# Kernel tuning notes

Measured on AMD Instinct MI355X. Metric: run time of the kernel, lower is better.

Reference implementation:

```python
import jax, jax.numpy as jnp
import numpy as np

D = 200          # in_feat == out_feat
N = 20000        # num nodes
E = 320000       # num edges
R = 512          # num relation types


def setup_inputs() -> dict:
    key = jax.random.key(0)
    ks = jax.random.split(key, 12)
    # glorot-ish init scale for params
    def glorot(k, shape):
        fan = shape[0] + shape[1]
        return jax.random.normal(k, shape, dtype=jnp.float32) * jnp.sqrt(2.0 / fan)
    return {
        "node": jax.random.normal(ks[0], (N, D), dtype=jnp.float32),
        "rel": jax.random.normal(ks[1], (R, D), dtype=jnp.float32),
        "norm": jax.random.uniform(ks[2], (N, 1), dtype=jnp.float32),
        "fre": jax.random.uniform(ks[3], (E,), dtype=jnp.float32),
        "w_triplet": glorot(ks[4], (3 * D, D)),
        "w_quad": glorot(ks[5], (D, D)),
        "loop_weight": glorot(ks[6], (D, D)),
        "evolve_loop_weight": glorot(ks[7], (D, D)),
        "edge_src": jax.random.randint(ks[8], (E,), 0, N, dtype=jnp.int64).astype(jnp.int32),
        "edge_dst": jax.random.randint(ks[9], (E,), 0, N, dtype=jnp.int64).astype(jnp.int32),
        "edge_type": jax.random.randint(ks[10], (E,), 0, R, dtype=jnp.int64).astype(jnp.int32),
    }


def reference(node, rel, norm, fre, w_triplet, w_quad, loop_weight,
              evolve_loop_weight, edge_src, edge_dst, edge_type):
    n = node.shape[0]
    d = node.shape[1]
    # gather per-edge features
    src_h = node[edge_src]            # [E, D]
    dst_h = node[edge_dst]            # [E, D]
    rel_emb = rel[edge_type]          # [E, D]
    # quads_msg_func: concat([src,rel,dst]) @ w_triplet, split to avoid [E,3D] concat
    W_s, W_r, W_d = w_triplet[:d], w_triplet[d:2 * d], w_triplet[2 * d:]
    triplet = src_h @ W_s + rel_emb @ W_r + dst_h @ W_d   # [E, D]
    a = (triplet + fre[:, None]) @ w_quad                 # [E, D]
    a = jax.nn.leaky_relu(a, negative_slope=0.01)
    # edge softmax over incoming edges per destination node (per channel)
    seg_max = jax.ops.segment_max(a, edge_dst, num_segments=n)   # [N, D]
    ex = jnp.exp(a - seg_max[edge_dst])
    seg_sum = jax.ops.segment_sum(ex, edge_dst, num_segments=n)  # [N, D]
    att = ex / seg_sum[edge_dst]
    # weighted message aggregation + per-node norm
    h = jax.ops.segment_sum(att * triplet, edge_dst, num_segments=n)
    h = h * norm
    # self-loop: loop_weight where in_degree > 0, else evolve_loop_weight
    deg = jax.ops.segment_sum(jnp.ones((edge_dst.shape[0],), dtype=jnp.float32),
                              edge_dst, num_segments=n)
    loop_msg = jnp.where((deg > 0)[:, None],
                         node @ loop_weight,
                         node @ evolve_loop_weight)
    return jax.nn.relu(h + loop_msg)
```

## Files before the change

### kernel.cpp

```cpp
#include <hip/hip_runtime.h>
#include <hip/hip_bf16.h>
#include <cstdint>
#include <cstddef>

#define DD 200
#define NN 20000
#define EE 320000
#define RRR 512
#define KP 256
#define KREAL 224
#define MT 157
#define NT 10
#define RMT 4
#define RNT 4
#define NBLK_NODE (MT * NT)

typedef __attribute__((ext_vector_type(8))) short bf16x8;
typedef __attribute__((ext_vector_type(4))) float f32x4;

__device__ __forceinline__ float bf2f_lo(unsigned int u) { return __uint_as_float(u << 16); }
__device__ __forceinline__ float bf2f_hi(unsigned int u) { return __uint_as_float(u & 0xffff0000u); }
__device__ __forceinline__ unsigned short f2bf(float f) {
  unsigned int x = __float_as_uint(f);
  return (unsigned short)((x + 0x7fffu + ((x >> 16) & 1u)) >> 16);
}
__device__ __forceinline__ unsigned int f2bf2(float a, float b) {
  return (unsigned int)f2bf(a) | ((unsigned int)f2bf(b) << 16);
}
__device__ __forceinline__ void gl_lds16(const unsigned short* g, unsigned short* l) {
  __builtin_amdgcn_global_load_lds(
      (const __attribute__((address_space(1))) void*)g,
      (__attribute__((address_space(3))) void*)l, 16, 0, 0);
}

__global__ __launch_bounds__(256) void kA(const float* __restrict__ wt, const float* __restrict__ wq,
                                          const float* __restrict__ lw, const float* __restrict__ elw,
                                          unsigned short* __restrict__ Bt,
                                          unsigned short* __restrict__ BtRel,
                                          float* __restrict__ cq, int* __restrict__ degcur) {
  int b = blockIdx.x, t = threadIdx.x;
  if (b < 200) {
    int k = b, j = t;
    if (j >= DD) return;
    const float* w0 = wt + (size_t)k * DD;
    const float* w1 = wt + (size_t)(2 * DD + k) * DD;
    const float* w2 = wt + (size_t)(DD + k) * DD;
    float s0 = 0.f, s1 = 0.f, s2 = 0.f;
    for (int i = 0; i < DD; ++i) {
      float q = wq[i * DD + j];
      s0 = fmaf(w0[i], q, s0);
      s1 = fmaf(w1[i], q, s1);
      s2 = fmaf(w2[i], q, s2);
    }
    Bt[(2 * j) * KP + k]       = f2bf(w0[j]);
    Bt[(2 * j + 1) * KP + k]   = f2bf(s0);
    Bt[(400 + 2 * j) * KP + k] = f2bf(w1[j]);
    Bt[(401 + 2 * j) * KP + k] = f2bf(s1);
    Bt[(800 + 2 * j) * KP + k] = f2bf(lw[k * DD + j]);
    Bt[(801 + 2 * j) * KP + k] = f2bf(elw[k * DD + j]);
    BtRel[(2 * j) * KP + k]     = f2bf(w2[j]);
    BtRel[(2 * j + 1) * KP + k] = f2bf(s2);
  } else if (b == 200) {
    int j = t; if (j >= DD) return;
    float s = 0.f;
    for (int i = 0; i < DD; ++i) s += wq[i * DD + j];
    cq[j] = s;
  } else if (b < 397) {
    int idx = (b - 201) * 256 + t;
    if (idx < 1792 * 28) {
      int col = idx / 28, kk = idx % 28;
      ((unsigned int*)Bt)[col * 128 + 100 + kk] = 0;
    }
  } else {
    int idx = (b - 397) * 256 + t;
    if (idx < 2 * NN) degcur[idx] = 0;
  }
}

__global__ __launch_bounds__(128) void k_prep(const float* __restrict__ node, const float* __restrict__ rel,
                                              const int* __restrict__ dst,
                                              unsigned int* __restrict__ Au, unsigned int* __restrict__ Arelu,
                                              int* __restrict__ deg) {
  int b = blockIdx.x, t = threadIdx.x;
  if (b < NN) {
    unsigned v = 0;
    if (t < 100) { float2 f = ((const float2*)(node + (size_t)b * DD))[t]; v = f2bf2(f.x, f.y); }
    Au[(size_t)b * 128 + t] = v;
  } else if (b < NN + RRR) {
    int r = b - NN; unsigned v = 0;
    if (t < 100) { float2 f = ((const float2*)(rel + (size_t)r * DD))[t]; v = f2bf2(f.x, f.y); }
    Arelu[(size_t)r * 128 + t] = v;
  } else {
    int e = (b - NN - RRR) * 128 + t;
    if (e < EE) atomicAdd(&deg[dst[e]], 1);
  }
}

__global__ __launch_bounds__(1024) void k_scan(const int* __restrict__ deg, int* __restrict__ offs) {
  __shared__ int wsum[16];
  __shared__ int carry_s;
  int tid = threadIdx.x, lane = tid & 63, wv = tid >> 6;
  if (tid == 0) carry_s = 0;
  __syncthreads();
  const int4* deg4 = (const int4*)deg;
  int4* offs4 = (int4*)offs;
  for (int base = 0; base < 5000; base += 1024) {
    int idx = base + tid;
    int4 v = make_int4(0, 0, 0, 0);
    if (idx < 5000) v = deg4[idx];
    int tsum = v.x + v.y + v.z + v.w;
    int x = tsum;
#pragma unroll
    for (int off = 1; off < 64; off <<= 1) {
      int y = __shfl_up(x, off, 64);
      if (lane >= off) x += y;
    }
    if (lane == 63) wsum[wv] = x;
    __syncthreads();
    if (wv == 0) {
      int w = (lane < 16) ? wsum[lane] : 0;
#pragma unroll
      for (int off = 1; off < 16; off <<= 1) {
        int y = __shfl_up(w, off, 64);
        if (lane >= off) w += y;
      }
      if (lane < 16) wsum[lane] = w;
    }
    __syncthreads();
    int pre = carry_s + ((wv > 0) ? wsum[wv - 1] : 0) + x - tsum;
    if (idx < 5000) {
      int a = pre, b = pre + v.x, c = b + v.y, d = c + v.z;
      offs4[idx] = make_int4(a, b, c, d);
    }
    __syncthreads();
    if (tid == 1023) carry_s += wsum[15];
    __syncthreads();
  }
  if (tid == 0) offs[NN] = carry_s;
}

__global__ __launch_bounds__(256) void k_gemm(const unsigned short* __restrict__ A,
                                              const unsigned short* __restrict__ Bt,
                                              unsigned short* __restrict__ NT2u,
                                              const unsigned short* __restrict__ Arel,
                                              const unsigned short* __restrict__ BtRel,
                                              unsigned short* __restrict__ RelPu) {
  __shared__ unsigned short As[128 * 32];
  __shared__ unsigned short Bs[128 * 32];
  bool isrel = blockIdx.x >= NBLK_NODE;
  int bid, ntn;
  const unsigned short *Ag, *Bg;
  if (!isrel) { bid = blockIdx.x; ntn = NT; Ag = A; Bg = Bt; }
  else        { bid = blockIdx.x - NBLK_NODE; ntn = RNT; Ag = Arel; Bg = BtRel; }
  int mt = bid / ntn, nt = bid % ntn;
  int t = threadIdx.x, lane = t & 63, wv = t >> 6;
  int lr = lane & 15, k8 = lane >> 4;
  int wm = (wv >> 1) * 64, wn = (wv & 1) * 64;
  int sr = wv * 16 + (lane >> 2);
  int sc = lane & 3;
  f32x4 acc[4][4] = {};
  Ag += (size_t)(mt * 128) * KP;
  Bg += (size_t)(nt * 128) * KP;
  for (int kk = 0; kk < KREAL; kk += 32) {
#pragma unroll
    for (int i = 0; i < 2; ++i) {
      int row = i * 64 + sr;
      int gcol = kk + ((sc ^ (row & 3)) << 3);
      gl_lds16(Ag + (size_t)row * KP + gcol, As + i * 2048 + wv * 512);
      gl_lds16(Bg + (size_t)row * KP + gcol, Bs + i * 2048 + wv * 512);
    }
    __syncthreads();
    bf16x8 af[4], bfr[4];
#pragma unroll
    for (int mi = 0; mi < 4; ++mi) {
      int row = wm + mi * 16 + lr;
      af[mi] = *(const bf16x8*)(As + row * 32 + ((k8 ^ (row & 3)) << 3));
      int col = wn + mi * 16 + lr;
      bfr[mi] = *(const bf16x8*)(Bs + col * 32 + ((k8 ^ (col & 3)) << 3));
    }
#pragma unroll
    for (int mi = 0; mi < 4; ++mi)
#pragma unroll
      for (int ni = 0; ni < 4; ++ni)
        acc[mi][ni] = __builtin_amdgcn_mfma_f32_16x16x32_bf16(af[mi], bfr[ni], acc[mi][ni], 0, 0, 0);
    __syncthreads();
  }
  int rb = k8 * 4;
#pragma unroll
  for (int mi = 0; mi < 4; ++mi)
#pragma unroll
    for (int ni = 0; ni < 4; ++ni) {
      int col = nt * 128 + wn + ni * 16 + lr;
      if (!isrel) {
        if (col < 1200) {
          int g = col / 400, w = col - g * 400;
          unsigned short* dst = NT2u + (size_t)g * NN * 400 + w;
#pragma unroll
          for (int r = 0; r < 4; ++r) {
            int row = mt * 128 + wm + mi * 16 + rb + r;
            if (row < NN) dst[(size_t)row * 400] = f2bf(acc[mi][ni][r]);
          }
        }
      } else {
        if (col < 400) {
#pragma unroll
          for (int r = 0; r < 4; ++r) {
            int row = mt * 128 + wm + mi * 16 + rb + r;
            RelPu[(size_t)row * 400 + col] = f2bf(acc[mi][ni][r]);
          }
        }
      }
    }
}

__global__ __launch_bounds__(256) void k_scatter(const int* __restrict__ src, const int* __restrict__ dst,
                                                 const int* __restrict__ typ, const float* __restrict__ fre,
                                                 const int* __restrict__ offs, int* __restrict__ cursor,
                                                 int* __restrict__ spk, float* __restrict__ sfre) {
  int e = blockIdx.x * 256 + threadIdx.x;
  if (e >= EE) return;
  int d = dst[e];
  int p = offs[d] + atomicAdd(&cursor[d], 1);
  spk[p] = src[e] | (typ[e] << 15);
  sfre[p] = fre[e];
}

__global__ __launch_bounds__(128) void k_agg(const uint2* __restrict__ GS2,
                                             const uint2* __restrict__ GD2,
                                             const uint2* __restrict__ GL2,
                                             const uint2* __restrict__ Rel2,
                                             const float2* __restrict__ cq2,
                                             const float* __restrict__ norm,
                                             const int* __restrict__ offs,
                                             const int* __restrict__ spk, const float* __restrict__ sfre,
                                             float* __restrict__ out) {
  int n = blockIdx.x;
  int j2 = threadIdx.x;
  if (j2 >= 100) return;
  int e0 = offs[n], e1 = offs[n + 1];
  uint2 dp = GD2[(size_t)n * 100 + j2];
  float xd0 = bf2f_lo(dp.x), xq0 = bf2f_hi(dp.x);
  float xd1 = bf2f_lo(dp.y), xq1 = bf2f_hi(dp.y);
  float2 cqv = cq2[j2];
  float s0 = 0.f, s1 = 0.f, num0 = 0.f, num1 = 0.f;
  int i = e0;
  for (; i + 4 <= e1; i += 4) {
    int p0 = spk[i], p1 = spk[i + 1], p2 = spk[i + 2], p3 = spk[i + 3];
    float f0 = sfre[i], f1 = sfre[i + 1], f2 = sfre[i + 2], f3 = sfre[i + 3];
    uint2 sA = GS2[((unsigned)p0 & 0x7fffu) * 100u + j2];
    uint2 sB = GS2[((unsigned)p1 & 0x7fffu) * 100u + j2];
    uint2 sC = GS2[((unsigned)p2 & 0x7fffu) * 100u + j2];
    uint2 sD = GS2[((unsigned)p3 & 0x7fffu) * 100u + j2];
    uint2 rA = Rel2[((unsigned)p0 >> 15) * 100u + j2];
    uint2 rB = Rel2[((unsigned)p1 >> 15) * 100u + j2];
    uint2 rC = Rel2[((unsigned)p2 >> 15) * 100u + j2];
    uint2 rD = Rel2[((unsigned)p3 >> 15) * 100u + j2];
#define DO_EDGE(SP, RP, F)                                                    \
    {                                                                         \
      float t0 = bf2f_lo(SP.x) + bf2f_lo(RP.x) + xd0;                         \
      float a0 = bf2f_hi(SP.x) + bf2f_hi(RP.x) + fmaf(F, cqv.x, xq0);         \
      float t1 = bf2f_lo(SP.y) + bf2f_lo(RP.y) + xd1;                         \
      float a1 = bf2f_hi(SP.y) + bf2f_hi(RP.y) + fmaf(F, cqv.y, xq1);         \
      a0 = fmaxf(a0, 0.01f * a0); a1 = fmaxf(a1, 0.01f * a1);                 \
      float ev0 = __expf(a0), ev1 = __expf(a1);                               \
      s0 += ev0; num0 = fmaf(ev0, t0, num0);                                  \
      s1 += ev1; num1 = fmaf(ev1, t1, num1);                                  \
    }
    DO_EDGE(sA, rA, f0)
    DO_EDGE(sB, rB, f1)
    DO_EDGE(sC, rC, f2)
    DO_EDGE(sD, rD, f3)
  }
  for (; i < e1; ++i) {
    int p = spk[i]; float f = sfre[i];
    uint2 sp = GS2[((unsigned)p & 0x7fffu) * 100u + j2];
    uint2 rp = Rel2[((unsigned)p >> 15) * 100u + j2];
    DO_EDGE(sp, rp, f)
  }
#undef DO_EDGE
  uint2 lp = GL2[(size_t)n * 100 + j2];
  float o0, o1;
  if (e1 > e0) {
    float nm = norm[n];
    o0 = (num0 / s0) * nm + bf2f_lo(lp.x);
    o1 = (num1 / s1) * nm + bf2f_lo(lp.y);
  } else {
    o0 = bf2f_hi(lp.x);
    o1 = bf2f_hi(lp.y);
  }
  ((float2*)(out + (size_t)n * DD))[j2] = make_float2(fmaxf(o0, 0.f), fmaxf(o1, 0.f));
}

extern "C" void kernel_launch(void* const* d_in, const int* in_sizes, int n_in,
                              void* d_out, int out_size, void* d_ws, size_t ws_size,
                              hipStream_t stream) {
  const float* node = (const float*)d_in[0];
  const float* rel  = (const float*)d_in[1];
  const float* norm = (const float*)d_in[2];
  const float* fre  = (const float*)d_in[3];
  const float* wt   = (const float*)d_in[4];
  const float* wq   = (const float*)d_in[5];
  const float* lw   = (const float*)d_in[6];
  const float* elw  = (const float*)d_in[7];
  const int* esrc = (const int*)d_in[8];
  const int* edst = (const int*)d_in[9];
  const int* etyp = (const int*)d_in[10];
  float* out = (float*)d_out;

  char* p = (char*)d_ws;
  auto carve = [&](size_t bytes) -> char* {
    char* r = p; p += (bytes + 255) & ~(size_t)255; return r;
  };
  unsigned short* A     = (unsigned short*)carve((size_t)(MT * 128) * KP * 2);
  unsigned short* Arel  = (unsigned short*)carve((size_t)RRR * KP * 2);
  unsigned short* BtAll = (unsigned short*)carve((size_t)(1280 + 512) * KP * 2);
  unsigned short* NT2   = (unsigned short*)carve((size_t)3 * NN * 400 * 2);
  unsigned short* RelP  = (unsigned short*)carve((size_t)RRR * 400 * 2);
  float* cq   = (float*)carve((size_t)DD * 4);
  int* degcur = (int*)carve((size_t)2 * NN * 4);
  int* offs   = (int*)carve((size_t)(NN + 1) * 4);
  int* spk    = (int*)carve((size_t)EE * 4);
  float* sfre = (float*)carve((size_t)EE * 4);

  unsigned short* Bt    = BtAll;
  unsigned short* BtRel = BtAll + (size_t)1280 * KP;
  int* deg    = degcur;
  int* cursor = degcur + NN;

  const uint2* GS2 = (const uint2*)NT2;
  const uint2* GD2 = GS2 + (size_t)NN * 100;
  const uint2* GL2 = GS2 + (size_t)2 * NN * 100;

  kA<<<554, 256, 0, stream>>>(wt, wq, lw, elw, Bt, BtRel, cq, degcur);
  k_prep<<<NN + RRR + (EE + 127) / 128, 128, 0, stream>>>(node, rel, edst,
                                                          (unsigned int*)A, (unsigned int*)Arel, deg);
  k_scan<<<1, 1024, 0, stream>>>(deg, offs);
  k_gemm<<<NBLK_NODE + RMT * RNT, 256, 0, stream>>>(A, Bt, NT2, Arel, BtRel, RelP);
  k_scatter<<<(EE + 255) / 256, 256, 0, stream>>>(esrc, edst, etyp, fre, offs, cursor,
                                                  spk, sfre);
  k_agg<<<NN, 128, 0, stream>>>(GS2, GD2, GL2, (const uint2*)RelP, (const float2*)cq,
                                norm, offs, spk, sfre, out);
}
```

Baseline: 144.1 us.

## Merge prep kernels, single-pass scan, pack edge records, deepen agg unroll

Merges the weight-prep and node/rel conversion kernels into one launch, with two rows per 256-thread block, and replaces the zeroing of degree counters with a memset. The scan now does a single pass, each thread handling five int4 chunks, instead of looping with a carried sum. Edge source/type and fre are packed into one int2 record. The aggregation loop is unrolled to 8 edges with all loads issued first to raise memory-level parallelism, and the constant dst term is pulled out of the per-edge sum. Scatter is also launched before the GEMM. This reduces launch count and serial scan latency, at the cost of more registers in the aggregation kernel.

```diff
diff --git a/kernel.cpp b/kernel.cpp
--- a/kernel.cpp
+++ b/kernel.cpp
@@ -15,6 +15,13 @@
 #define RNT 4
 #define NBLK_NODE (MT * NT)
 
+#define PB_NODE 10000
+#define PB_REL  (PB_NODE + 256)
+#define PB_HIST (PB_REL + 1250)
+#define PB_W    (PB_HIST + 200)
+#define PB_CQ   (PB_W + 1)
+#define PB_PAD  (PB_CQ + 196)
+
 typedef __attribute__((ext_vector_type(8))) short bf16x8;
 typedef __attribute__((ext_vector_type(4))) float f32x4;
 
@@ -33,14 +40,32 @@
       (__attribute__((address_space(3))) void*)l, 16, 0, 0);
 }
 
-__global__ __launch_bounds__(256) void kA(const float* __restrict__ wt, const float* __restrict__ wq,
-                                          const float* __restrict__ lw, const float* __restrict__ elw,
-                                          unsigned short* __restrict__ Bt,
-                                          unsigned short* __restrict__ BtRel,
-                                          float* __restrict__ cq, int* __restrict__ degcur) {
+__global__ __launch_bounds__(256) void kPrep(const float* __restrict__ node, const float* __restrict__ rel,
+                                             const int* __restrict__ dst,
+                                             const float* __restrict__ wt, const float* __restrict__ wq,
+                                             const float* __restrict__ lw, const float* __restrict__ elw,
+                                             unsigned int* __restrict__ Au, unsigned int* __restrict__ Arelu,
+                                             int* __restrict__ deg,
+                                             unsigned short* __restrict__ Bt, unsigned short* __restrict__ BtRel,
+                                             float* __restrict__ cq) {
   int b = blockIdx.x, t = threadIdx.x;
-  if (b < 200) {
-    int k = b, j = t;
+  if (b < PB_NODE) {
+    int h = t >> 7, tt = t & 127;
+    int n = b * 2 + h;
+    unsigned v = 0;
+    if (tt < 100) { float2 f = ((const float2*)(node + (size_t)n * DD))[tt]; v = f2bf2(f.x, f.y); }
+    Au[(size_t)n * 128 + tt] = v;
+  } else if (b < PB_REL) {
+    int h = t >> 7, tt = t & 127;
+    int r = (b - PB_NODE) * 2 + h;
+    unsigned v = 0;
+    if (tt < 100) { float2 f = ((const float2*)(rel + (size_t)r * DD))[tt]; v = f2bf2(f.x, f.y); }
+    Arelu[(size_t)r * 128 + tt] = v;
+  } else if (b < PB_HIST) {
+    int e = (b - PB_REL) * 256 + t;
+    if (e < EE) atomicAdd(&deg[dst[e]], 1);
+  } else if (b < PB_W) {
+    int k = b - PB_HIST, j = t;
     if (j >= DD) return;
     const float* w0 = wt + (size_t)k * DD;
     const float* w1 = wt + (size_t)(2 * DD + k) * DD;
@@ -60,83 +85,59 @@
     Bt[(801 + 2 * j) * KP + k] = f2bf(elw[k * DD + j]);
     BtRel[(2 * j) * KP + k]     = f2bf(w2[j]);
     BtRel[(2 * j + 1) * KP + k] = f2bf(s2);
-  } else if (b == 200) {
+  } else if (b < PB_CQ) {
     int j = t; if (j >= DD) return;
     float s = 0.f;
     for (int i = 0; i < DD; ++i) s += wq[i * DD + j];
     cq[j] = s;
-  } else if (b < 397) {
-    int idx = (b - 201) * 256 + t;
-    if (idx < 1792 * 28) {
-      int col = idx / 28, kk = idx % 28;
-      ((unsigned int*)Bt)[col * 128 + 100 + kk] = 0;
-    }
   } else {
-    int idx = (b - 397) * 256 + t;
-    if (idx < 2 * NN) degcur[idx] = 0;
-  }
-}
-
-__global__ __launch_bounds__(128) void k_prep(const float* __restrict__ node, const float* __restrict__ rel,
-                                              const int* __restrict__ dst,
-                                              unsigned int* __restrict__ Au, unsigned int* __restrict__ Arelu,
-                                              int* __restrict__ deg) {
-  int b = blockIdx.x, t = threadIdx.x;
-  if (b < NN) {
-    unsigned v = 0;
-    if (t < 100) { float2 f = ((const float2*)(node + (size_t)b * DD))[t]; v = f2bf2(f.x, f.y); }
-    Au[(size_t)b * 128 + t] = v;
-  } else if (b < NN + RRR) {
-    int r = b - NN; unsigned v = 0;
-    if (t < 100) { float2 f = ((const float2*)(rel + (size_t)r * DD))[t]; v = f2bf2(f.x, f.y); }
-    Arelu[(size_t)r * 128 + t] = v;
-  } else {
-    int e = (b - NN - RRR) * 128 + t;
-    if (e < EE) atomicAdd(&deg[dst[e]], 1);
+    int idx = (b - PB_CQ) * 256 + t;
+    ((unsigned int*)Bt)[(idx / 28) * 128 + 100 + idx % 28] = 0;
   }
 }
 
 __global__ __launch_bounds__(1024) void k_scan(const int* __restrict__ deg, int* __restrict__ offs) {
   __shared__ int wsum[16];
-  __shared__ int carry_s;
   int tid = threadIdx.x, lane = tid & 63, wv = tid >> 6;
-  if (tid == 0) carry_s = 0;
-  __syncthreads();
   const int4* deg4 = (const int4*)deg;
   int4* offs4 = (int4*)offs;
-  for (int base = 0; base < 5000; base += 1024) {
-    int idx = base + tid;
-    int4 v = make_int4(0, 0, 0, 0);
-    if (idx < 5000) v = deg4[idx];
-    int tsum = v.x + v.y + v.z + v.w;
-    int x = tsum;
-#pragma unroll
-    for (int off = 1; off < 64; off <<= 1) {
-      int y = __shfl_up(x, off, 64);
-      if (lane >= off) x += y;
-    }
-    if (lane == 63) wsum[wv] = x;
-    __syncthreads();
-    if (wv == 0) {
-      int w = (lane < 16) ? wsum[lane] : 0;
-#pragma unroll
-      for (int off = 1; off < 16; off <<= 1) {
-        int y = __shfl_up(w, off, 64);
-        if (lane >= off) w += y;
-      }
-      if (lane < 16) wsum[lane] = w;
-    }
-    __syncthreads();
-    int pre = carry_s + ((wv > 0) ? wsum[wv - 1] : 0) + x - tsum;
+  int4 v[5]; int ps[5]; int tsum = 0;
+#pragma unroll
+  for (int c = 0; c < 5; ++c) {
+    int idx = tid * 5 + c;
+    v[c] = (idx < 5000) ? deg4[idx] : make_int4(0, 0, 0, 0);
+    ps[c] = tsum;
+    tsum += v[c].x + v[c].y + v[c].z + v[c].w;
+  }
+  int x = tsum;
+#pragma unroll
+  for (int off = 1; off < 64; off <<= 1) {
+    int y = __shfl_up(x, off, 64);
+    if (lane >= off) x += y;
+  }
+  if (lane == 63) wsum[wv] = x;
+  __syncthreads();
+  if (wv == 0) {
+    int w = (lane < 16) ? wsum[lane] : 0;
+#pragma unroll
+    for (int off = 1; off < 16; off <<= 1) {
+      int y = __shfl_up(w, off, 64);
+      if (lane >= off) w += y;
+    }
+    if (lane < 16) wsum[lane] = w;
+  }
+  __syncthreads();
+  int pre = ((wv > 0) ? wsum[wv - 1] : 0) + x - tsum;
+#pragma unroll
+  for (int c = 0; c < 5; ++c) {
+    int idx = tid * 5 + c;
     if (idx < 5000) {
-      int a = pre, b = pre + v.x, c = b + v.y, d = c + v.z;
-      offs4[idx] = make_int4(a, b, c, d);
-    }
-    __syncthreads();
-    if (tid == 1023) carry_s += wsum[15];
-    __syncthreads();
-  }
-  if (tid == 0) offs[NN] = carry_s;
+      int a = pre + ps[c];
+      int bq = a + v[c].x, cc = bq + v[c].y, d = cc + v[c].z;
+      offs4[idx] = make_int4(a, bq, cc, d);
+    }
+  }
+  if (tid == 0) offs[NN] = wsum[15];
 }
 
 __global__ __launch_bounds__(256) void k_gemm(const unsigned short* __restrict__ A,
@@ -216,13 +217,12 @@
 __global__ __launch_bounds__(256) void k_scatter(const int* __restrict__ src, const int* __restrict__ dst,
                                                  const int* __restrict__ typ, const float* __restrict__ fre,
                                                  const int* __restrict__ offs, int* __restrict__ cursor,
-                                                 int* __restrict__ spk, float* __restrict__ sfre) {
+                                                 int2* __restrict__ erec) {
   int e = blockIdx.x * 256 + threadIdx.x;
   if (e >= EE) return;
   int d = dst[e];
   int p = offs[d] + atomicAdd(&cursor[d], 1);
-  spk[p] = src[e] | (typ[e] << 15);
-  sfre[p] = fre[e];
+  erec[p] = make_int2(src[e] | (typ[e] << 15), __float_as_int(fre[e]));
 }
 
 __global__ __launch_bounds__(128) void k_agg(const uint2* __restrict__ GS2,
@@ -232,7 +232,7 @@
                                              const float2* __restrict__ cq2,
                                              const float* __restrict__ norm,
                                              const int* __restrict__ offs,
-                                             const int* __restrict__ spk, const float* __restrict__ sfre,
+                                             const int2* __restrict__ erec,
                                              float* __restrict__ out) {
   int n = blockIdx.x;
   int j2 = threadIdx.x;
@@ -243,47 +243,55 @@
   float xd1 = bf2f_lo(dp.y), xq1 = bf2f_hi(dp.y);
   float2 cqv = cq2[j2];
   float s0 = 0.f, s1 = 0.f, num0 = 0.f, num1 = 0.f;
+#define DO_EDGE(SP, RP, FI)                                                   \
+  {                                                                           \
+    float F = __int_as_float(FI);                                             \
+    float t0 = bf2f_lo(SP.x) + bf2f_lo(RP.x);                                 \
+    float a0 = bf2f_hi(SP.x) + bf2f_hi(RP.x) + fmaf(F, cqv.x, xq0);           \
+    float t1 = bf2f_lo(SP.y) + bf2f_lo(RP.y);                                 \
+    float a1 = bf2f_hi(SP.y) + bf2f_hi(RP.y) + fmaf(F, cqv.y, xq1);           \
+    a0 = fmaxf(a0, 0.01f * a0); a1 = fmaxf(a1, 0.01f * a1);                   \
+    float ev0 = __expf(a0), ev1 = __expf(a1);                                 \
+    s0 += ev0; num0 = fmaf(ev0, t0, num0);                                    \
+    s1 += ev1; num1 = fmaf(ev1, t1, num1);                                    \
+  }
   int i = e0;
-  for (; i + 4 <= e1; i += 4) {
-    int p0 = spk[i], p1 = spk[i + 1], p2 = spk[i + 2], p3 = spk[i + 3];
-    float f0 = sfre[i], f1 = sfre[i + 1], f2 = sfre[i + 2], f3 = sfre[i + 3];
-    uint2 sA = GS2[((unsigned)p0 & 0x7fffu) * 100u + j2];
-    uint2 sB = GS2[((unsigned)p1 & 0x7fffu) * 100u + j2];
-    uint2 sC = GS2[((unsigned)p2 & 0x7fffu) * 100u + j2];
-    uint2 sD = GS2[((unsigned)p3 & 0x7fffu) * 100u + j2];
-    uint2 rA = Rel2[((unsigned)p0 >> 15) * 100u + j2];
-    uint2 rB = Rel2[((unsigned)p1 >> 15) * 100u + j2];
-    uint2 rC = Rel2[((unsigned)p2 >> 15) * 100u + j2];
-    uint2 rD = Rel2[((unsigned)p3 >> 15) * 100u + j2];
-#define DO_EDGE(SP, RP, F)                                                    \
-    {                                                                         \
-      float t0 = bf2f_lo(SP.x) + bf2f_lo(RP.x) + xd0;                         \
-      float a0 = bf2f_hi(SP.x) + bf2f_hi(RP.x) + fmaf(F, cqv.x, xq0);         \
-      float t1 = bf2f_lo(SP.y) + bf2f_lo(RP.y) + xd1;                         \
-      float a1 = bf2f_hi(SP.y) + bf2f_hi(RP.y) + fmaf(F, cqv.y, xq1);         \
-      a0 = fmaxf(a0, 0.01f * a0); a1 = fmaxf(a1, 0.01f * a1);                 \
-      float ev0 = __expf(a0), ev1 = __expf(a1);                               \
-      s0 += ev0; num0 = fmaf(ev0, t0, num0);                                  \
-      s1 += ev1; num1 = fmaf(ev1, t1, num1);                                  \
-    }
-    DO_EDGE(sA, rA, f0)
-    DO_EDGE(sB, rB, f1)
-    DO_EDGE(sC, rC, f2)
-    DO_EDGE(sD, rD, f3)
+  for (; i + 8 <= e1; i += 8) {
+    int2 r[8]; uint2 g[8], R[8];
+#pragma unroll
+    for (int u = 0; u < 8; ++u) r[u] = erec[i + u];
+#pragma unroll
+    for (int u = 0; u < 8; ++u) g[u] = GS2[((unsigned)r[u].x & 0x7fffu) * 100u + j2];
+#pragma unroll
+    for (int u = 0; u < 8; ++u) R[u] = Rel2[((unsigned)r[u].x >> 15) * 100u + j2];
+#pragma unroll
+    for (int u = 0; u < 8; ++u) DO_EDGE(g[u], R[u], r[u].y)
+  }
+  if (i + 4 <= e1) {
+    int2 r[4]; uint2 g[4], R[4];
+#pragma unroll
+    for (int u = 0; u < 4; ++u) r[u] = erec[i + u];
+#pragma unroll
+    for (int u = 0; u < 4; ++u) g[u] = GS2[((unsigned)r[u].x & 0x7fffu) * 100u + j2];
+#pragma unroll
+    for (int u = 0; u < 4; ++u) R[u] = Rel2[((unsigned)r[u].x >> 15) * 100u + j2];
+#pragma unroll
+    for (int u = 0; u < 4; ++u) DO_EDGE(g[u], R[u], r[u].y)
+    i += 4;
   }
   for (; i < e1; ++i) {
-    int p = spk[i]; float f = sfre[i];
-    uint2 sp = GS2[((unsigned)p & 0x7fffu) * 100u + j2];
-    uint2 rp = Rel2[((unsigned)p >> 15) * 100u + j2];
-    DO_EDGE(sp, rp, f)
+    int2 r = erec[i];
+    uint2 g = GS2[((unsigned)r.x & 0x7fffu) * 100u + j2];
+    uint2 R = Rel2[((unsigned)r.x >> 15) * 100u + j2];
+    DO_EDGE(g, R, r.y)
   }
 #undef DO_EDGE
   uint2 lp = GL2[(size_t)n * 100 + j2];
   float o0, o1;
   if (e1 > e0) {
     float nm = norm[n];
-    o0 = (num0 / s0) * nm + bf2f_lo(lp.x);
-    o1 = (num1 / s1) * nm + bf2f_lo(lp.y);
+    o0 = (num0 / s0 + xd0) * nm + bf2f_lo(lp.x);
+    o1 = (num1 / s1 + xd1) * nm + bf2f_lo(lp.y);
   } else {
     o0 = bf2f_hi(lp.x);
     o1 = bf2f_hi(lp.y);
@@ -319,8 +327,7 @@
   float* cq   = (float*)carve((size_t)DD * 4);
   int* degcur = (int*)carve((size_t)2 * NN * 4);
   int* offs   = (int*)carve((size_t)(NN + 1) * 4);
-  int* spk    = (int*)carve((size_t)EE * 4);
-  float* sfre = (float*)carve((size_t)EE * 4);
+  int2* erec  = (int2*)carve((size_t)EE * 8);
 
   unsigned short* Bt    = BtAll;
   unsigned short* BtRel = BtAll + (size_t)1280 * KP;
@@ -331,13 +338,12 @@
   const uint2* GD2 = GS2 + (size_t)NN * 100;
   const uint2* GL2 = GS2 + (size_t)2 * NN * 100;
 
-  kA<<<554, 256, 0, stream>>>(wt, wq, lw, elw, Bt, BtRel, cq, degcur);
-  k_prep<<<NN + RRR + (EE + 127) / 128, 128, 0, stream>>>(node, rel, edst,
-                                                          (unsigned int*)A, (unsigned int*)Arel, deg);
+  hipMemsetAsync(degcur, 0, (size_t)2 * NN * 4, stream);
+  kPrep<<<PB_PAD, 256, 0, stream>>>(node, rel, edst, wt, wq, lw, elw,
+                                    (unsigned int*)A, (unsigned int*)Arel, deg, Bt, BtRel, cq);
   k_scan<<<1, 1024, 0, stream>>>(deg, offs);
+  k_scatter<<<(EE + 255) / 256, 256, 0, stream>>>(esrc, edst, etyp, fre, offs, cursor, erec);
   k_gemm<<<NBLK_NODE + RMT * RNT, 256, 0, stream>>>(A, Bt, NT2, Arel, BtRel, RelP);
-  k_scatter<<<(EE + 255) / 256, 256, 0, stream>>>(esrc, edst, etyp, fre, offs, cursor,
-                                                  spk, sfre);
   k_agg<<<NN, 128, 0, stream>>>(GS2, GD2, GL2, (const uint2*)RelP, (const float2*)cq,
-                                norm, offs, spk, sfre, out);
-}
+                                norm, offs, erec, out);
+}
```

Result: no change. 142.3 us (-1.3%).
